# Performance work log

Measured on AMD Instinct MI355X. Metric: run time of the kernel, lower is better.

## Reference

```python
import jax, jax.numpy as jnp
import numpy as np

W_CD = 1.0   # cfg TRAIN.LOSS_WEIGHT_CHAMFER_DISTANCE
W_RV = 1.0   # cfg TRAIN.LOSS_WEIGHT_RANGE_VIEW
W_MASK = 1.0 # cfg TRAIN.LOSS_WEIGHT_MASK


def setup_inputs() -> dict:
    key = jax.random.key(0)
    k0, k1, k2, k3, k4 = jax.random.split(key, 5)
    B, T, H, W = 2, 5, 64, 2048   # batch, future steps, range-image dims
    N = M = 4096                  # n_samples (TEST.N_DOWNSAMPLED_POINTS_CD)
    output_rv = jax.random.normal(k0, (B, T, H, W), jnp.float32)
    mask_logits = jax.random.normal(k1, (B, T, H, W), jnp.float32)
    target_range_image = jax.random.normal(k2, (B, T, H, W), jnp.float32)
    output_points = jax.random.normal(k3, (B, T, N, 3), jnp.float32)
    target_points = jax.random.normal(k4, (B, T, M, 3), jnp.float32)
    return {
        "output_rv": output_rv,
        "mask_logits": mask_logits,
        "output_points": output_points,
        "target_points": target_points,
        "target_range_image": target_range_image,
    }


def _chamfer(output_points, target_points):
    on = jnp.sum(output_points * output_points, axis=-1)            # [B,T,N]
    tn = jnp.sum(target_points * target_points, axis=-1)            # [B,T,M]
    cross = jnp.einsum('btnd,btmd->btnm', output_points, target_points)
    d2 = on[..., :, None] + tn[..., None, :] - 2.0 * cross          # [B,T,N,M]
    dist1 = jnp.min(d2, axis=-1).mean(axis=-1)                      # [B,T] out->tgt NN
    dist2 = jnp.min(d2, axis=-2).mean(axis=-1)                      # [B,T] tgt->out NN
    cd_bt = dist1 + dist2                                           # per (b,s) CD
    return cd_bt.T, jnp.mean(cd_bt)                                 # [T,B] tensor, scalar mean


def reference(output_rv, mask_logits, output_points, target_points, target_range_image):
    # L1 range loss: output values are forced to -1 wherever target == -1
    out_m = jnp.where(target_range_image == -1.0, -1.0, output_rv)
    loss_rv = jnp.mean(jnp.abs(out_m - target_range_image))
    # mask BCE-with-logits: target mask is 1 where range view is valid (> 0)
    tmask = (target_range_image > 0.0).astype(output_rv.dtype)
    x = mask_logits
    loss_mask = jnp.mean(jnp.maximum(x, 0.0) - x * tmask + jnp.log1p(jnp.exp(-jnp.abs(x))))
    # Chamfer distance over fixed-size subsampled point clouds
    cd_tensor, loss_cd = _chamfer(output_points, target_points)
    total = W_CD * loss_cd + W_RV * loss_rv + W_MASK * loss_mask
    return total, cd_tensor, loss_cd, loss_rv, loss_mask
```

## Files before the change

kernel.cpp:

```cpp
#include <hip/hip_runtime.h>
#include <math.h>

#define BB 2
#define TT 5
#define NPTS 4096
#define NBT (BB * TT)
#define NELEM (BB * TT * 64 * 2048)

#define CH_BLOCKS 640
#define QPB 128
#define NQC (NPTS / QPB)
#define CT 1024
#define NT (NPTS / CT)
#define EW_BLOCKS 640

#define EW1 2560
#define EW2 3200

typedef _Float16 h8 __attribute__((ext_vector_type(8)));
typedef float f32x16 __attribute__((ext_vector_type(16)));
typedef float f32x4 __attribute__((ext_vector_type(4)));

__device__ inline unsigned pkh(float a, float b) {
    union { _Float16 h[2]; unsigned u; } c;
    c.h[0] = (_Float16)a;
    c.h[1] = (_Float16)b;
    return c.u;
}

__global__ __launch_bounds__(256) void main_kernel(
        const float4* __restrict__ rv4,
        const float4* __restrict__ lg4,
        const float4* __restrict__ tg4,
        const float* __restrict__ OP,
        const float* __restrict__ TP,
        float* __restrict__ ws) {
    __shared__ __align__(16) uint2 pts[2][CT];
    __shared__ float nqlds[4][32];
    int bid = blockIdx.x;
    int tid = threadIdx.x;
    int lane = tid & 63;
    int wave = tid >> 6;

    if (bid >= CH_BLOCKS) {
        int eb = bid - CH_BLOCKS;
        float srv = 0.0f, smk = 0.0f;
        int base = (eb * 256 + tid) * 2;
#pragma unroll
        for (int u = 0; u < 2; ++u) {
            int i = base + u;
            float4 o4 = rv4[i];
            float4 x4 = lg4[i];
            float4 t4 = tg4[i];
            const float* op = &o4.x;
            const float* xp = &x4.x;
            const float* tp = &t4.x;
#pragma unroll
            for (int j = 0; j < 4; ++j) {
                float tv = tp[j];
                float ov = (tv == -1.0f) ? -1.0f : op[j];
                srv += fabsf(ov - tv);
                float tm = (tv > 0.0f) ? 1.0f : 0.0f;
                float xv = xp[j];
                smk += fmaxf(xv, 0.0f) - xv * tm + __logf(1.0f + __expf(-fabsf(xv)));
            }
        }
#pragma unroll
        for (int off = 32; off > 0; off >>= 1) {
            srv += __shfl_down(srv, off);
            smk += __shfl_down(smk, off);
        }
        __shared__ float s1[4], s2[4];
        if (lane == 0) { s1[wave] = srv; s2[wave] = smk; }
        __syncthreads();
        if (tid == 0) {
            ws[EW1 + eb] = s1[0] + s1[1] + s1[2] + s1[3];
            ws[EW2 + eb] = s2[0] + s2[1] + s2[2] + s2[3];
        }
        return;
    }

    int dir = bid / (NBT * NQC);
    int rem = bid % (NBT * NQC);
    int bt = rem / NQC;
    int qc = rem % NQC;
    const float* P = dir ? TP : OP;
    const float* Q = dir ? OP : TP;
    const float* Pb = P + (size_t)bt * NPTS * 3;
    const float* Qb = Q + (size_t)bt * NPTS * 3;

    int qrow = lane & 31;
    int qidx = qc * QPB + wave * 32 + qrow;
    float qx = 0.0f, qy = 0.0f, qz = 0.0f;
    if (lane < 32) {
        const float* p = Pb + (size_t)qidx * 3;
        qx = p[0]; qy = p[1]; qz = p[2];
        nqlds[wave][qrow] = fmaf(qx, qx, fmaf(qy, qy, qz * qz));
    }
    union { unsigned u[4]; h8 h; } ua;
    ua.u[0] = ua.u[1] = ua.u[2] = ua.u[3] = 0u;
    if (lane < 32) {
        ua.u[0] = pkh(-2.0f * qx, -2.0f * qy);
        ua.u[1] = pkh(-2.0f * qz, 1.0f);
    }
    h8 afrag = ua.h;

    const f32x16 zc = {0.0f, 0.0f, 0.0f, 0.0f, 0.0f, 0.0f, 0.0f, 0.0f,
                       0.0f, 0.0f, 0.0f, 0.0f, 0.0f, 0.0f, 0.0f, 0.0f};
    float vm[16];
#pragma unroll
    for (int r = 0; r < 16; ++r) vm[r] = INFINITY;

#define STAGE(t, b)                                                          \
    {                                                                        \
        int pt0 = (t) * CT + tid * 4;                                        \
        const f32x4* src = (const f32x4*)(Qb + (size_t)pt0 * 3);             \
        f32x4 c0 = src[0], c1 = src[1], c2 = src[2];                         \
        float x0 = c0[0], y0 = c0[1], z0 = c0[2];                            \
        float x1 = c0[3], y1 = c1[0], z1 = c1[1];                            \
        float x2 = c1[2], y2 = c1[3], z2 = c2[0];                            \
        float x3 = c2[1], y3 = c2[2], z3 = c2[3];                            \
        float n0 = fmaf(x0, x0, fmaf(y0, y0, z0 * z0));                      \
        float n1 = fmaf(x1, x1, fmaf(y1, y1, z1 * z1));                      \
        float n2 = fmaf(x2, x2, fmaf(y2, y2, z2 * z2));                      \
        float n3 = fmaf(x3, x3, fmaf(y3, y3, z3 * z3));                      \
        uint4* dst = (uint4*)&pts[b][tid * 4];                               \
        dst[0] = make_uint4(pkh(x0, y0), pkh(z0, n0), pkh(x1, y1), pkh(z1, n1)); \
        dst[1] = make_uint4(pkh(x2, y2), pkh(z2, n2), pkh(x3, y3), pkh(z3, n3)); \
    }

    STAGE(0, 0);
    __syncthreads();
    for (int t = 0; t < NT; ++t) {
        if (t + 1 < NT) STAGE(t + 1, (t + 1) & 1);
        const uint2* pb = pts[t & 1];
#pragma unroll 2
        for (int s = 0; s < CT / 64; ++s) {
            uint2 b0 = make_uint2(0u, 0u), b1 = make_uint2(0u, 0u);
            if (lane < 32) {
                b0 = pb[s * 64 + qrow];
                b1 = pb[s * 64 + 32 + qrow];
            }
            union { unsigned u[4]; h8 h; } ub0, ub1;
            ub0.u[0] = b0.x; ub0.u[1] = b0.y; ub0.u[2] = 0u; ub0.u[3] = 0u;
            ub1.u[0] = b1.x; ub1.u[1] = b1.y; ub1.u[2] = 0u; ub1.u[3] = 0u;
            f32x16 d0 = __builtin_amdgcn_mfma_f32_32x32x16_f16(afrag, ub0.h, zc, 0, 0, 0);
            f32x16 d1 = __builtin_amdgcn_mfma_f32_32x32x16_f16(afrag, ub1.h, zc, 0, 0, 0);
#pragma unroll
            for (int r = 0; r < 16; ++r) {
                float a = d0[r], c = d1[r];
                asm("v_min3_f32 %0, %0, %1, %2" : "+v"(vm[r]) : "v"(a), "v"(c));
            }
        }
        __syncthreads();
    }

#pragma unroll
    for (int r = 0; r < 16; ++r) {
        float m = vm[r];
        m = fminf(m, __shfl_xor(m, 1));
        m = fminf(m, __shfl_xor(m, 2));
        m = fminf(m, __shfl_xor(m, 4));
        m = fminf(m, __shfl_xor(m, 8));
        m = fminf(m, __shfl_xor(m, 16));
        vm[r] = m;
    }
    float part = 0.0f;
    if ((lane & 31) == 0) {
        int half = lane >> 5;
#pragma unroll
        for (int r = 0; r < 16; ++r) {
            int row = (r & 3) + 8 * (r >> 2) + 4 * half;
            part += vm[r] + nqlds[wave][row];
        }
    }
    part += __shfl_xor(part, 32);
    if (lane == 0) ws[bid * 4 + wave] = part;
}

__global__ void finalize_kernel(const float* __restrict__ ws, float* __restrict__ out) {
    __shared__ float grp[20];
    __shared__ float ra[4], rb[4];
    int tid = threadIdx.x;
    int lane = tid & 63;
    int wave = tid >> 6;

    for (int g = wave; g < 20; g += 4) {
        float s = 0.0f;
        for (int j = lane; j < 128; j += 64) s += ws[g * 128 + j];
#pragma unroll
        for (int off = 32; off > 0; off >>= 1) s += __shfl_down(s, off);
        if (lane == 0) grp[g] = s;
    }

    float sa = 0.0f, sb = 0.0f;
    for (int i = tid; i < EW_BLOCKS; i += 256) {
        sa += ws[EW1 + i];
        sb += ws[EW2 + i];
    }
#pragma unroll
    for (int off = 32; off > 0; off >>= 1) {
        sa += __shfl_down(sa, off);
        sb += __shfl_down(sb, off);
    }
    if (lane == 0) { ra[wave] = sa; rb[wave] = sb; }
    __syncthreads();

    if (tid == 0) {
        const float inv_e = 1.0f / (float)NELEM;
        float loss_rv = (ra[0] + ra[1] + ra[2] + ra[3]) * inv_e;
        float loss_mask = (rb[0] + rb[1] + rb[2] + rb[3]) * inv_e;
        float cd_sum = 0.0f;
        for (int bt = 0; bt < NBT; ++bt) {
            float cd = (grp[bt] + grp[NBT + bt]) * (1.0f / NPTS);
            int b = bt / TT;
            int t = bt % TT;
            out[1 + t * BB + b] = cd;
            cd_sum += cd;
        }
        float loss_cd = cd_sum / (float)NBT;
        out[0] = loss_cd + loss_rv + loss_mask;
        out[11] = loss_cd;
        out[12] = loss_rv;
        out[13] = loss_mask;
    }
}

extern "C" void kernel_launch(void* const* d_in, const int* in_sizes, int n_in,
                              void* d_out, int out_size, void* d_ws, size_t ws_size,
                              hipStream_t stream) {
    const float* output_rv = (const float*)d_in[0];
    const float* mask_logits = (const float*)d_in[1];
    const float* output_points = (const float*)d_in[2];
    const float* target_points = (const float*)d_in[3];
    const float* target_rv = (const float*)d_in[4];
    float* out = (float*)d_out;
    float* ws = (float*)d_ws;

    main_kernel<<<CH_BLOCKS + EW_BLOCKS, 256, 0, stream>>>(
        (const float4*)output_rv, (const float4*)mask_logits,
        (const float4*)target_rv, output_points, target_points, ws);

    finalize_kernel<<<1, 256, 0, stream>>>(ws, out);
}
```

Measured before the change: 34.02 us.

## Split chamfer candidate range across two blocks and add per-query min-combine kernel

Each chamfer block now scans only half of the candidate points (tiles ph and ph+2), which doubles the chamfer grid to 1280 blocks and gives the GPU more independent work. Blocks write per-query partial minima to workspace, and a new combine kernel takes the min of the two halves and sums per (dir, bt) group. The inner loop is unrolled to four MFMAs per group, the lane<32 guard on the LDS loads is dropped, and the elementwise blocks are placed first in the grid. The cost is an extra kernel launch and more workspace traffic.

Result: no change. 34.05 us (+0.1%).

```diff
diff --git a/kernel.cpp b/kernel.cpp
--- a/kernel.cpp
+++ b/kernel.cpp
@@ -7,15 +7,15 @@
 #define NBT (BB * TT)
 #define NELEM (BB * TT * 64 * 2048)
 
-#define CH_BLOCKS 640
+#define EW_BLOCKS 640
+#define CH_BLOCKS 1280
 #define QPB 128
-#define NQC (NPTS / QPB)
+#define NQC 32
 #define CT 1024
-#define NT (NPTS / CT)
-#define EW_BLOCKS 640
-
-#define EW1 2560
-#define EW2 3200
+
+#define GRP 163840
+#define EW1 163860
+#define EW2 164500
 
 typedef _Float16 h8 __attribute__((ext_vector_type(8)));
 typedef float f32x16 __attribute__((ext_vector_type(16)));
@@ -42,10 +42,9 @@
     int lane = tid & 63;
     int wave = tid >> 6;
 
-    if (bid >= CH_BLOCKS) {
-        int eb = bid - CH_BLOCKS;
+    if (bid < EW_BLOCKS) {
         float srv = 0.0f, smk = 0.0f;
-        int base = (eb * 256 + tid) * 2;
+        int base = (bid * 256 + tid) * 2;
 #pragma unroll
         for (int u = 0; u < 2; ++u) {
             int i = base + u;
@@ -74,16 +73,19 @@
         if (lane == 0) { s1[wave] = srv; s2[wave] = smk; }
         __syncthreads();
         if (tid == 0) {
-            ws[EW1 + eb] = s1[0] + s1[1] + s1[2] + s1[3];
-            ws[EW2 + eb] = s2[0] + s2[1] + s2[2] + s2[3];
+            ws[EW1 + bid] = s1[0] + s1[1] + s1[2] + s1[3];
+            ws[EW2 + bid] = s2[0] + s2[1] + s2[2] + s2[3];
         }
         return;
     }
 
-    int dir = bid / (NBT * NQC);
-    int rem = bid % (NBT * NQC);
-    int bt = rem / NQC;
-    int qc = rem % NQC;
+    int cb = bid - EW_BLOCKS;
+    int dir = cb / 640;
+    int rem = cb % 640;
+    int bt = rem / 64;
+    int r2 = rem % 64;
+    int qc = r2 >> 1;
+    int ph = r2 & 1;
     const float* P = dir ? TP : OP;
     const float* Q = dir ? OP : TP;
     const float* Pb = P + (size_t)bt * NPTS * 3;
@@ -129,31 +131,43 @@
         dst[1] = make_uint4(pkh(x2, y2), pkh(z2, n2), pkh(x3, y3), pkh(z3, n3)); \
     }
 
-    STAGE(0, 0);
-    __syncthreads();
-    for (int t = 0; t < NT; ++t) {
-        if (t + 1 < NT) STAGE(t + 1, (t + 1) & 1);
-        const uint2* pb = pts[t & 1];
-#pragma unroll 2
-        for (int s = 0; s < CT / 64; ++s) {
-            uint2 b0 = make_uint2(0u, 0u), b1 = make_uint2(0u, 0u);
-            if (lane < 32) {
-                b0 = pb[s * 64 + qrow];
-                b1 = pb[s * 64 + 32 + qrow];
-            }
-            union { unsigned u[4]; h8 h; } ub0, ub1;
-            ub0.u[0] = b0.x; ub0.u[1] = b0.y; ub0.u[2] = 0u; ub0.u[3] = 0u;
-            ub1.u[0] = b1.x; ub1.u[1] = b1.y; ub1.u[2] = 0u; ub1.u[3] = 0u;
-            f32x16 d0 = __builtin_amdgcn_mfma_f32_32x32x16_f16(afrag, ub0.h, zc, 0, 0, 0);
-            f32x16 d1 = __builtin_amdgcn_mfma_f32_32x32x16_f16(afrag, ub1.h, zc, 0, 0, 0);
-#pragma unroll
-            for (int r = 0; r < 16; ++r) {
-                float a = d0[r], c = d1[r];
-                asm("v_min3_f32 %0, %0, %1, %2" : "+v"(vm[r]) : "v"(a), "v"(c));
-            }
-        }
-        __syncthreads();
-    }
+#define COMPUTE(buf)                                                         \
+    {                                                                        \
+        const uint2* pb = pts[buf];                                          \
+        _Pragma("unroll")                                                    \
+        for (int g = 0; g < CT / 128; ++g) {                                 \
+            uint2 b0 = pb[g * 128 + 0 * 32 + qrow];                          \
+            uint2 b1 = pb[g * 128 + 1 * 32 + qrow];                          \
+            uint2 b2 = pb[g * 128 + 2 * 32 + qrow];                          \
+            uint2 b3 = pb[g * 128 + 3 * 32 + qrow];                          \
+            union { unsigned u[4]; h8 h; } ub0, ub1, ub2, ub3;               \
+            ub0.u[0] = b0.x; ub0.u[1] = b0.y; ub0.u[2] = 0u; ub0.u[3] = 0u;  \
+            ub1.u[0] = b1.x; ub1.u[1] = b1.y; ub1.u[2] = 0u; ub1.u[3] = 0u;  \
+            ub2.u[0] = b2.x; ub2.u[1] = b2.y; ub2.u[2] = 0u; ub2.u[3] = 0u;  \
+            ub3.u[0] = b3.x; ub3.u[1] = b3.y; ub3.u[2] = 0u; ub3.u[3] = 0u;  \
+            f32x16 d0 = __builtin_amdgcn_mfma_f32_32x32x16_f16(afrag, ub0.h, zc, 0, 0, 0); \
+            f32x16 d1 = __builtin_amdgcn_mfma_f32_32x32x16_f16(afrag, ub1.h, zc, 0, 0, 0); \
+            f32x16 d2 = __builtin_amdgcn_mfma_f32_32x32x16_f16(afrag, ub2.h, zc, 0, 0, 0); \
+            f32x16 d3 = __builtin_amdgcn_mfma_f32_32x32x16_f16(afrag, ub3.h, zc, 0, 0, 0); \
+            _Pragma("unroll")                                                \
+            for (int r = 0; r < 16; ++r) {                                   \
+                float a = d0[r], c = d1[r];                                  \
+                asm("v_min3_f32 %0, %0, %1, %2" : "+v"(vm[r]) : "v"(a), "v"(c)); \
+            }                                                                \
+            _Pragma("unroll")                                                \
+            for (int r = 0; r < 16; ++r) {                                   \
+                float a = d2[r], c = d3[r];                                  \
+                asm("v_min3_f32 %0, %0, %1, %2" : "+v"(vm[r]) : "v"(a), "v"(c)); \
+            }                                                                \
+        }                                                                    \
+    }
+
+    STAGE(ph, 0);
+    __syncthreads();
+    STAGE(ph + 2, 1);
+    COMPUTE(0);
+    __syncthreads();
+    COMPUTE(1);
 
 #pragma unroll
     for (int r = 0; r < 16; ++r) {
@@ -165,33 +179,42 @@
         m = fminf(m, __shfl_xor(m, 16));
         vm[r] = m;
     }
-    float part = 0.0f;
+    size_t qbase = ((size_t)(dir * NBT + bt) * NQC + qc) * 256 + ph * QPB + wave * 32;
     if ((lane & 31) == 0) {
         int half = lane >> 5;
 #pragma unroll
         for (int r = 0; r < 16; ++r) {
             int row = (r & 3) + 8 * (r >> 2) + 4 * half;
-            part += vm[r] + nqlds[wave][row];
-        }
-    }
-    part += __shfl_xor(part, 32);
-    if (lane == 0) ws[bid * 4 + wave] = part;
+            ws[qbase + row] = vm[r] + nqlds[wave][row];
+        }
+    }
+}
+
+__global__ void combine_kernel(const float* __restrict__ ws, float* __restrict__ wso) {
+    __shared__ float sred[4];
+    int g = blockIdx.x;
+    int tid = threadIdx.x;
+    int lane = tid & 63;
+    int wave = tid >> 6;
+    float s = 0.0f;
+    for (int j = tid; j < NPTS; j += 256) {
+        int qcv = j >> 7;
+        int i = j & 127;
+        const float* b = ws + ((size_t)g * NQC + qcv) * 256 + i;
+        s += fminf(b[0], b[QPB]);
+    }
+#pragma unroll
+    for (int off = 32; off > 0; off >>= 1) s += __shfl_down(s, off);
+    if (lane == 0) sred[wave] = s;
+    __syncthreads();
+    if (tid == 0) wso[GRP + g] = sred[0] + sred[1] + sred[2] + sred[3];
 }
 
 __global__ void finalize_kernel(const float* __restrict__ ws, float* __restrict__ out) {
-    __shared__ float grp[20];
     __shared__ float ra[4], rb[4];
     int tid = threadIdx.x;
     int lane = tid & 63;
     int wave = tid >> 6;
-
-    for (int g = wave; g < 20; g += 4) {
-        float s = 0.0f;
-        for (int j = lane; j < 128; j += 64) s += ws[g * 128 + j];
-#pragma unroll
-        for (int off = 32; off > 0; off >>= 1) s += __shfl_down(s, off);
-        if (lane == 0) grp[g] = s;
-    }
 
     float sa = 0.0f, sb = 0.0f;
     for (int i = tid; i < EW_BLOCKS; i += 256) {
@@ -212,7 +235,7 @@
         float loss_mask = (rb[0] + rb[1] + rb[2] + rb[3]) * inv_e;
         float cd_sum = 0.0f;
         for (int bt = 0; bt < NBT; ++bt) {
-            float cd = (grp[bt] + grp[NBT + bt]) * (1.0f / NPTS);
+            float cd = (ws[GRP + bt] + ws[GRP + NBT + bt]) * (1.0f / NPTS);
             int b = bt / TT;
             int t = bt % TT;
             out[1 + t * BB + b] = cd;
@@ -237,9 +260,11 @@
     float* out = (float*)d_out;
     float* ws = (float*)d_ws;
 
-    main_kernel<<<CH_BLOCKS + EW_BLOCKS, 256, 0, stream>>>(
+    main_kernel<<<EW_BLOCKS + CH_BLOCKS, 256, 0, stream>>>(
         (const float4*)output_rv, (const float4*)mask_logits,
         (const float4*)target_rv, output_points, target_points, ws);
 
+    combine_kernel<<<20, 256, 0, stream>>>(ws, ws);
+
     finalize_kernel<<<1, 256, 0, stream>>>(ws, out);
 }
```
